# Kernel tuning notes

Measured on AMD Instinct MI355X. Metric: run time of the kernel, lower is better.

## Reference

```python
import jax, jax.numpy as jnp
import numpy as np
import math

D_INNER = 512
D_STATE = 16
DT_RANK = 32
B_SZ = 2
L_SEQ = 4096


def setup_inputs() -> dict:
    key = jax.random.key(0)
    ks = jax.random.split(key, 6)
    x = jax.random.normal(ks[0], (B_SZ, L_SEQ, D_INNER), dtype=jnp.float32)
    # parameters (match torch init semantics closely enough for a numeric baseline)
    A = jnp.arange(1, D_STATE + 1, dtype=jnp.float32)
    A_log = jnp.broadcast_to(jnp.log(A)[None, :], (D_INNER, D_STATE)).copy()
    D_param = jnp.ones((D_INNER,), dtype=jnp.float32)
    # x_proj: Linear(d_inner -> dt_rank + 2*d_state), no bias
    W_xproj = jax.random.normal(ks[1], (DT_RANK + 2 * D_STATE, D_INNER), dtype=jnp.float32) / np.sqrt(D_INNER)
    # dt_proj: Linear(dt_rank -> d_inner) with special bias init
    W_dt = jax.random.normal(ks[2], (D_INNER, DT_RANK), dtype=jnp.float32) / np.sqrt(DT_RANK)
    dt_init = jnp.exp(jax.random.uniform(ks[3], (D_INNER,)) * (math.log(0.1) - math.log(0.001)) + math.log(0.001))
    b_dt = jnp.log(jnp.exp(dt_init) - 1.0)
    alpha = jnp.asarray(0.6, dtype=jnp.float32)
    beta_logit = jnp.asarray(math.log(0.99 / (1.0 - 0.99 + 1e-08)), dtype=jnp.float32)
    return {"x": x, "A_log": A_log, "D_param": D_param, "W_xproj": W_xproj,
            "W_dt": W_dt, "b_dt": b_dt, "alpha": alpha, "beta_logit": beta_logit}


def _momentum_ssm(x, A_log, D_param, W_xproj, W_dt, b_dt, alpha, beta_logit):
    # x: (B, L, D)
    proj = jnp.einsum('bld,pd->blp', x, W_xproj)            # (B, L, r+2N)
    dt_in = proj[..., :DT_RANK]
    Bp = proj[..., DT_RANK:DT_RANK + D_STATE]                # (B, L, N)
    Cp = proj[..., DT_RANK + D_STATE:]                       # (B, L, N)
    dt = jax.nn.softplus(jnp.einsum('blr,dr->bld', dt_in, W_dt) + b_dt)  # (B, L, D)
    A = -jnp.exp(A_log)                                      # (D, N)
    A_bar = jnp.exp(dt[..., None] * A[None, None])           # (B, L, D, N)
    # fused B_bar * x_t: dt * Bp * x
    inp = dt[..., None] * Bp[:, :, None, :] * x[..., None]   # (B, L, D, N)
    beta = jax.nn.sigmoid(beta_logit)

    # scan over time; carry (h, v): (B, D, N)
    h0 = jnp.zeros((x.shape[0], D_INNER, D_STATE), dtype=x.dtype)
    v0 = jnp.zeros_like(h0)

    def step(carry, ts):
        h, v = carry
        a_t, inp_t, c_t = ts                                 # (B,D,N), (B,D,N), (B,N)
        v = beta * v + alpha * inp_t
        h = a_t * h + v
        y = jnp.einsum('bdn,bn->bd', h, c_t)
        return (h, v), y

    xs = (jnp.moveaxis(A_bar, 1, 0), jnp.moveaxis(inp, 1, 0), jnp.moveaxis(Cp, 1, 0))
    _, ys = jax.lax.scan(step, (h0, v0), xs)                 # ys: (L, B, D)
    y = jnp.moveaxis(ys, 0, 1)                               # (B, L, D)
    return y + D_param * x


def reference(x, A_log, D_param, W_xproj, W_dt, b_dt, alpha, beta_logit):
    return _momentum_ssm(x, A_log, D_param, W_xproj, W_dt, b_dt, alpha, beta_logit)
```

## Files before the change

kernel.cpp:

```cpp
#include <hip/hip_runtime.h>


#define D_IN 512
#define D_ST 16
#define DTR  32
#define BSZ  2
#define LSEQ 4096
#define PDIM 64
#define NCH  256
#define LCH  (LSEQ / NCH)
#define LOG2E 1.44269504f
#define LN2   0.69314718f

typedef __attribute__((ext_vector_type(8))) short short8;
typedef __attribute__((ext_vector_type(4))) float f32x4;
typedef _Float16 f16;
typedef __attribute__((ext_vector_type(8))) _Float16 f16x8;

__device__ inline float fast_exp2(float x) { return __builtin_amdgcn_exp2f(x); }
__device__ inline float fast_log2(float x) { return __builtin_amdgcn_logf(x); }

__device__ inline unsigned short bf16_rne(float f) {
  unsigned b = __float_as_uint(f);
  return (unsigned short)((b + 0x7fffu + ((b >> 16) & 1u)) >> 16);
}

__device__ inline void cvt8(const float4 u, const float4 v, short8& hi, short8& lo) {
  float f[8] = {u.x, u.y, u.z, u.w, v.x, v.y, v.z, v.w};
#pragma unroll
  for (int i = 0; i < 8; ++i) {
    unsigned short h = bf16_rne(f[i]);
    hi[i] = (short)h;
    float r = f[i] - __uint_as_float((unsigned)h << 16);
    lo[i] = (short)bf16_rne(r);
  }
}

__device__ inline void st16h(f16* p, const float* s) {
  f16 t[16];
#pragma unroll
  for (int i = 0; i < 16; ++i) t[i] = (f16)s[i];
  *(f16x8*)p = *(f16x8*)&t[0];
  *(f16x8*)(p + 8) = *(f16x8*)&t[8];
}
__device__ inline void ld16h(const f16* p, float* d) {
  f16x8 a = *(const f16x8*)p;
  f16x8 b = *(const f16x8*)(p + 8);
#pragma unroll
  for (int i = 0; i < 8; ++i) { d[i] = (float)a[i]; d[8 + i] = (float)b[i]; }
}

__device__ inline bool loadA2(const float* A_log, int d, float* A2) {
  const float4* ap = (const float4*)(A_log + (size_t)d * D_ST);
#pragma unroll
  for (int i = 0; i < 4; ++i) {
    float4 a4 = ap[i];
    A2[4 * i + 0] = -__expf(a4.x) * LOG2E;
    A2[4 * i + 1] = -__expf(a4.y) * LOG2E;
    A2[4 * i + 2] = -__expf(a4.z) * LOG2E;
    A2[4 * i + 3] = -__expf(a4.w) * LOG2E;
  }
  bool pw = true;
#pragma unroll
  for (int n = 1; n < 16; ++n) {
    float ref = (float)(n + 1) * A2[0];
    pw = pw && (fabsf(A2[n] - ref) <= 2e-5f * fabsf(ref));
  }
  return pw;
}

__global__ __launch_bounds__(256) void k_wprep(const float* __restrict__ W,
                                               short* __restrict__ Whi,
                                               short* __restrict__ Wlo) {
  const int i = (blockIdx.x * 256 + threadIdx.x) * 4;
  float4 w = *(const float4*)(W + i);
  float f[4] = {w.x, w.y, w.z, w.w};
  unsigned short h[4], lo[4];
#pragma unroll
  for (int j = 0; j < 4; ++j) {
    h[j] = bf16_rne(f[j]);
    float r = f[j] - __uint_as_float((unsigned)h[j] << 16);
    lo[j] = bf16_rne(r);
  }
  *(uint2*)(Whi + i) = make_uint2(h[0] | ((unsigned)h[1] << 16), h[2] | ((unsigned)h[3] << 16));
  *(uint2*)(Wlo + i) = make_uint2(lo[0] | ((unsigned)lo[1] << 16), lo[2] | ((unsigned)lo[3] << 16));
}

#define MM3(ACC, AH, AL, BH, BL)                                        \
  ACC = __builtin_amdgcn_mfma_f32_16x16x32_bf16(AL, BH, ACC, 0, 0, 0);  \
  ACC = __builtin_amdgcn_mfma_f32_16x16x32_bf16(AH, BL, ACC, 0, 0, 0);  \
  ACC = __builtin_amdgcn_mfma_f32_16x16x32_bf16(AH, BH, ACC, 0, 0, 0);

#define LOADB(P, S)                                   \
  {                                                   \
    const int kb = ((S) & 15) * 32;                   \
    P##h0 = *(const short8*)(bh + kb);                \
    P##h1 = *(const short8*)(bh + 8192 + kb);         \
    P##h2 = *(const short8*)(bh + 16384 + kb);        \
    P##h3 = *(const short8*)(bh + 24576 + kb);        \
    P##l0 = *(const short8*)(bl + kb);                \
    P##l1 = *(const short8*)(bl + 8192 + kb);         \
    P##l2 = *(const short8*)(bl + 16384 + kb);        \
    P##l3 = *(const short8*)(bl + 24576 + kb);        \
  }

#define LOADA(Aa, Ab, S)                              \
  {                                                   \
    const int ka = ((S) & 15) * 32;                   \
    Aa = *(const float4*)(xr + ka);                   \
    Ab = *(const float4*)(xr + ka + 4);               \
  }

#define SUBSTEP(Aa, Ab, P, SA, SB)                    \
  {                                                   \
    short8 ahi, alo;                                  \
    cvt8(Aa, Ab, ahi, alo);                           \
    MM3(acc0, ahi, alo, P##h0, P##l0);                \
    MM3(acc1, ahi, alo, P##h1, P##l1);                \
    MM3(acc2, ahi, alo, P##h2, P##l2);                \
    MM3(acc3, ahi, alo, P##h3, P##l3);                \
    LOADB(P, SB);                                     \
    LOADA(Aa, Ab, SA);                                \
  }

__global__ __launch_bounds__(64) void k_proj(const float* __restrict__ x,
                                             const short* __restrict__ Whi,
                                             const short* __restrict__ Wlo,
                                             float* __restrict__ proj) {
  const int row0 = blockIdx.x * 16;
  const int l = threadIdx.x;
  const int m = l & 15;
  const int ko = (l >> 4) * 8;
  const float* xr = x + (size_t)(row0 + m) * D_IN + ko;
  const short* bh = Whi + (size_t)m * D_IN + ko;
  const short* bl = Wlo + (size_t)m * D_IN + ko;

  f32x4 acc0 = {0.f, 0.f, 0.f, 0.f}, acc1 = acc0, acc2 = acc0, acc3 = acc0;
  float4 A0a, A0b, A1a, A1b, A2a, A2b, A3a, A3b;
  short8 Xh0, Xh1, Xh2, Xh3, Xl0, Xl1, Xl2, Xl3;
  short8 Yh0, Yh1, Yh2, Yh3, Yl0, Yl1, Yl2, Yl3;
  LOADA(A0a, A0b, 0); LOADA(A1a, A1b, 1); LOADA(A2a, A2b, 2); LOADA(A3a, A3b, 3);
  LOADB(X, 0); LOADB(Y, 1);

#pragma unroll
  for (int it = 0; it < 4; ++it) {
    const int s = it * 4;
    SUBSTEP(A0a, A0b, X, s + 4, s + 2);
    SUBSTEP(A1a, A1b, Y, s + 5, s + 3);
    SUBSTEP(A2a, A2b, X, s + 6, s + 4);
    SUBSTEP(A3a, A3b, Y, s + 7, s + 5);
  }

  const int r0 = (l >> 4) * 4;
#pragma unroll
  for (int r = 0; r < 4; ++r) {
    float* pr = proj + (size_t)(row0 + r0 + r) * PDIM + m;
    pr[0] = acc0[r]; pr[16] = acc1[r]; pr[32] = acc2[r]; pr[48] = acc3[r];
  }
}

#define S1_BODY(GET_A)                                        \
  _Pragma("unroll")                                           \
  for (int j = 0; j < LCH; ++j) {                             \
    const float dtc = dtv[j], xv = xs[j];                     \
    sd += dtc;                                                \
    bpow *= beta;                                             \
    const float u = alpha * dtc * xv;                         \
    GET_A;                                                    \
    float4 Bq[4];                                             \
    _Pragma("unroll")                                         \
    for (int i = 0; i < 4; ++i) Bq[i] = ((const float4*)&Ps[j][DTR])[i]; \
    const float* Bf = (const float*)Bq;                       \
    float ar = 1.f;                                           \
    _Pragma("unroll")                                         \
    for (int n = 0; n < 16; ++n) {                            \
      NEXT_A(ar, n);                                          \
      v[n] = fmaf(beta, v[n], u * Bf[n]);                     \
      h[n] = fmaf(ar, h[n], v[n]);                            \
      cv[n] = fmaf(ar, cv[n], bpow);                          \
    }                                                         \
  }

__global__ __launch_bounds__(256) void k_scan1(const float* __restrict__ x,
                                               const float* __restrict__ proj,
                                               const float* __restrict__ A_log,
                                               const float* __restrict__ W_dt,
                                               const float* __restrict__ b_dt,
                                               const float* __restrict__ alpha_p,
                                               const float* __restrict__ beta_p,
                                               f16* __restrict__ hh,
                                               f16* __restrict__ vh,
                                               f16* __restrict__ cvv,
                                               float* __restrict__ sdt,
                                               f16* __restrict__ dth) {
  __shared__ float Ps[LCH][PDIM];
  const int c = blockIdx.x, b = blockIdx.z;
  const int d = blockIdx.y * 256 + threadIdx.x;
  const int t0 = c * LCH;
  {
    const float4* src = (const float4*)(proj + ((size_t)b * LSEQ + t0) * PDIM);
    ((float4*)&Ps[0][0])[threadIdx.x] = src[threadIdx.x];
  }
  float xs[LCH];
  {
    const float* xp = x + ((size_t)b * LSEQ + t0) * D_IN + d;
#pragma unroll
    for (int j = 0; j < LCH; ++j) xs[j] = xp[(size_t)j * D_IN];
  }
  const float alpha = alpha_p[0];
  const float beta = 1.f / (1.f + __expf(-beta_p[0]));
  float A2[D_ST];
  const bool powA = loadA2(A_log, d, A2);
  __syncthreads();

  float dtv[LCH];
  {
    float4 w4[8];
    const float4* wp = (const float4*)(W_dt + (size_t)d * DTR);
#pragma unroll
    for (int i = 0; i < 8; ++i) w4[i] = wp[i];
    const float bb = b_dt[d];
#pragma unroll
    for (int j = 0; j < LCH; ++j) {
      const float4* pj = (const float4*)&Ps[j][0];
      float a0 = bb, a1 = 0.f, a2 = 0.f, a3 = 0.f;
#pragma unroll
      for (int k = 0; k < 8; ++k) {
        float4 p = pj[k];
        a0 = fmaf(p.x, w4[k].x, a0);
        a1 = fmaf(p.y, w4[k].y, a1);
        a2 = fmaf(p.z, w4[k].z, a2);
        a3 = fmaf(p.w, w4[k].w, a3);
      }
      float acc = (a0 + a1) + (a2 + a3);
      float e = fast_exp2(acc * LOG2E);
      dtv[j] = (acc > 20.f) ? acc : LN2 * fast_log2(1.f + e);
    }
  }
  {
    f16* dp = dth + ((size_t)b * LSEQ + t0) * D_IN + d;
#pragma unroll
    for (int j = 0; j < LCH; ++j) dp[(size_t)j * D_IN] = (f16)dtv[j];
  }

  float h[16] = {}, v[16] = {}, cv[16] = {};
  float bpow = 1.f, sd = 0.f;
  if (powA) {
#define NEXT_A(ar, n) ar *= r
    S1_BODY(const float r = fast_exp2(dtc * A2[0]))
#undef NEXT_A
  } else {
#define NEXT_A(ar, n) ar = fast_exp2(dtc * A2[n])
    S1_BODY()
#undef NEXT_A
  }

  const size_t base = ((size_t)(b * NCH + c) * D_IN + d) * D_ST;
  st16h(hh + base, h);
  st16h(vh + base, v);
  st16h(cvv + base, cv);
  sdt[(size_t)(b * NCH + c) * D_IN + d] = sd;
}

__global__ __launch_bounds__(64) void k_fix(f16* __restrict__ hh,
                                            f16* __restrict__ vh,
                                            const f16* __restrict__ cvv,
                                            const float* __restrict__ sdt,
                                            const float* __restrict__ A_log,
                                            const float* __restrict__ beta_p) {
  const int g = blockIdx.x * 64 + threadIdx.x;
  const int b = g >> 13;
  const int dn = g & 8191;
  const float beta = 1.f / (1.f + __expf(-beta_p[0]));
  const float A2 = -__expf(A_log[dn]) * LOG2E;
  float bL = beta;
#pragma unroll
  for (int i = 0; i < 4; ++i) bL *= bL;

  const size_t cs = (size_t)D_IN * D_ST;
  const size_t base = (size_t)b * NCH * cs + dn;
  const size_t sbase = (size_t)b * NCH * D_IN + (dn >> 4);

  float hg[8], vg[8], cg[8], sg[8];
#pragma unroll
  for (int i = 0; i < 8; ++i) {
    hg[i] = (float)hh[base + i * cs];
    vg[i] = (float)vh[base + i * cs];
    cg[i] = (float)cvv[base + i * cs];
    sg[i] = sdt[sbase + i * D_IN];
  }
  float H = 0.f, V = 0.f;
  for (int c0 = 0; c0 < NCH; c0 += 8) {
    const int cp = (c0 + 8) & (NCH - 1);
    float hn[8], vn[8], cn[8], sn[8];
#pragma unroll
    for (int i = 0; i < 8; ++i) {
      hn[i] = (float)hh[base + (size_t)(cp + i) * cs];
      vn[i] = (float)vh[base + (size_t)(cp + i) * cs];
      cn[i] = (float)cvv[base + (size_t)(cp + i) * cs];
      sn[i] = sdt[sbase + (size_t)(cp + i) * D_IN];
    }
#pragma unroll
    for (int i = 0; i < 8; ++i) {
      hh[base + (size_t)(c0 + i) * cs] = (f16)H;
      vh[base + (size_t)(c0 + i) * cs] = (f16)V;
      const float Pa = fast_exp2(sg[i] * A2);
      const float Hn = fmaf(Pa, H, fmaf(cg[i], V, hg[i]));
      V = fmaf(bL, V, vg[i]);
      H = Hn;
    }
#pragma unroll
    for (int i = 0; i < 8; ++i) { hg[i] = hn[i]; vg[i] = vn[i]; cg[i] = cn[i]; sg[i] = sn[i]; }
  }
}

#define S2_BODY(GET_A)                                        \
  _Pragma("unroll")                                           \
  for (int j = 0; j < LCH; ++j) {                             \
    const float dtc = dtv[j], xv = xs[j];                     \
    const float u = alpha * dtc * xv;                         \
    GET_A;                                                    \
    float4 Bq[8];                                             \
    _Pragma("unroll")                                         \
    for (int i = 0; i < 8; ++i) Bq[i] = ((const float4*)&Ps[j][DTR])[i]; \
    const float* Bf = (const float*)Bq;                       \
    float y0 = 0.f, y1 = 0.f, y2 = 0.f, y3 = 0.f;             \
    float ar = 1.f;                                           \
    _Pragma("unroll")                                         \
    for (int n = 0; n < 16; ++n) {                            \
      NEXT_A(ar, n);                                          \
      v[n] = fmaf(beta, v[n], u * Bf[n]);                     \
      h[n] = fmaf(ar, h[n], v[n]);                            \
      float hc = h[n] * Bf[16 + n];                           \
      if ((n & 3) == 0) y0 += hc;                             \
      else if ((n & 3) == 1) y1 += hc;                        \
      else if ((n & 3) == 2) y2 += hc;                        \
      else y3 += hc;                                          \
    }                                                         \
    op[(size_t)j * D_IN] = (y0 + y1) + (y2 + y3) + Dv * xv;   \
  }

__global__ __launch_bounds__(256) void k_scan2(const float* __restrict__ x,
                                               const f16* __restrict__ dth,
                                               const float* __restrict__ proj,
                                               const float* __restrict__ A_log,
                                               const float* __restrict__ D_param,
                                               const float* __restrict__ alpha_p,
                                               const float* __restrict__ beta_p,
                                               const f16* __restrict__ hh,
                                               const f16* __restrict__ vh,
                                               float* __restrict__ out) {
  __shared__ float Ps[LCH][PDIM];
  const int c = blockIdx.x, b = blockIdx.z;
  const int d = blockIdx.y * 256 + threadIdx.x;
  const int t0 = c * LCH;
  {
    const float4* src = (const float4*)(proj + ((size_t)b * LSEQ + t0) * PDIM);
    ((float4*)&Ps[0][0])[threadIdx.x] = src[threadIdx.x];
  }
  float xs[LCH], dtv[LCH];
  {
    const float* xp = x + ((size_t)b * LSEQ + t0) * D_IN + d;
    const f16* dp = dth + ((size_t)b * LSEQ + t0) * D_IN + d;
#pragma unroll
    for (int j = 0; j < LCH; ++j) xs[j] = xp[(size_t)j * D_IN];
#pragma unroll
    for (int j = 0; j < LCH; ++j) dtv[j] = (float)dp[(size_t)j * D_IN];
  }
  const float alpha = alpha_p[0];
  const float beta = 1.f / (1.f + __expf(-beta_p[0]));
  const float Dv = D_param[d];
  float A2[D_ST];
  const bool powA = loadA2(A_log, d, A2);
  const size_t ibase = ((size_t)(b * NCH + c) * D_IN + d) * D_ST;
  float h[16], v[16];
  ld16h(hh + ibase, h);
  ld16h(vh + ibase, v);
  __syncthreads();

  float* op = out + ((size_t)b * LSEQ + t0) * D_IN + d;
  if (powA) {
#define NEXT_A(ar, n) ar *= r
    S2_BODY(const float r = fast_exp2(dtc * A2[0]))
#undef NEXT_A
  } else {
#define NEXT_A(ar, n) ar = fast_exp2(dtc * A2[n])
    S2_BODY()
#undef NEXT_A
  }
}

extern "C" void kernel_launch(void* const* d_in, const int* in_sizes, int n_in,
                              void* d_out, int out_size, void* d_ws, size_t ws_size,
                              hipStream_t stream) {
  const float* x = (const float*)d_in[0];
  const float* A_log = (const float*)d_in[1];
  const float* D_param = (const float*)d_in[2];
  const float* W_xproj = (const float*)d_in[3];
  const float* W_dt = (const float*)d_in[4];
  const float* b_dt = (const float*)d_in[5];
  const float* alpha = (const float*)d_in[6];
  const float* beta_logit = (const float*)d_in[7];
  float* out = (float*)d_out;

  const size_t NST = (size_t)BSZ * NCH * D_IN * D_ST;
  float* ws = (float*)d_ws;
  float* proj = ws;
  float* sdt = proj + (size_t)BSZ * LSEQ * PDIM;
  f16* hh = (f16*)(sdt + (size_t)BSZ * NCH * D_IN);
  f16* vh = hh + NST;
  f16* cvv = vh + NST;
  f16* dth = cvv + NST;
  short* Whi = (short*)(dth + (size_t)BSZ * LSEQ * D_IN);
  short* Wlo = Whi + (size_t)PDIM * D_IN;

  k_wprep<<<dim3(PDIM * D_IN / 1024), dim3(256), 0, stream>>>(W_xproj, Whi, Wlo);
  k_proj<<<dim3(BSZ * LSEQ / 16), dim3(64), 0, stream>>>(x, Whi, Wlo, proj);
  k_scan1<<<dim3(NCH, D_IN / 256, BSZ), dim3(256), 0, stream>>>(
      x, proj, A_log, W_dt, b_dt, alpha, beta_logit, hh, vh, cvv, sdt, dth);
  k_fix<<<dim3(BSZ * D_IN * D_ST / 64), dim3(64), 0, stream>>>(hh, vh, cvv, sdt, A_log,
                                                               beta_logit);
  k_scan2<<<dim3(NCH, D_IN / 256, BSZ), dim3(256), 0, stream>>>(
      x, dth, proj, A_log, D_param, alpha, beta_logit, hh, vh, out);
}
```

Baseline: 172.5 us.

## Move dt projection into a separate MFMA kernel with split-bf16 weights

The dt = softplus(dt_in·W_dtᵀ + b) computation moves out of the scan1 per-thread FMA loop into a new k_dt kernel. That kernel uses bf16 hi/lo split MFMAs, with W_dt prepared in k_wprep. scan1 now reads dt from the f16 buffer, and both scans stage only the B/C columns into smaller shared arrays, with launch bounds asking for 4 blocks per CU. This removes the scalar GEMV work from the latency-bound scan and may raise occupancy. In exchange it adds a kernel launch plus a global write and read of dt.

```diff
diff --git a/kernel.cpp b/kernel.cpp
--- a/kernel.cpp
+++ b/kernel.cpp
@@ -17,6 +17,9 @@
 typedef _Float16 f16;
 typedef __attribute__((ext_vector_type(8))) _Float16 f16x8;
 
+__device__ __align__(16) short g_Wdh[D_IN * DTR];
+__device__ __align__(16) short g_Wdl[D_IN * DTR];
+
 __device__ inline float fast_exp2(float x) { return __builtin_amdgcn_exp2f(x); }
 __device__ inline float fast_log2(float x) { return __builtin_amdgcn_logf(x); }
 
@@ -70,10 +73,19 @@
 }
 
 __global__ __launch_bounds__(256) void k_wprep(const float* __restrict__ W,
+                                               const float* __restrict__ Wdt,
                                                short* __restrict__ Whi,
                                                short* __restrict__ Wlo) {
   const int i = (blockIdx.x * 256 + threadIdx.x) * 4;
-  float4 w = *(const float4*)(W + i);
+  const float* src;
+  short *dh, *dl;
+  if (i < PDIM * D_IN) {
+    src = W + i; dh = Whi + i; dl = Wlo + i;
+  } else {
+    const int k = i - PDIM * D_IN;
+    src = Wdt + k; dh = g_Wdh + k; dl = g_Wdl + k;
+  }
+  float4 w = *(const float4*)src;
   float f[4] = {w.x, w.y, w.z, w.w};
   unsigned short h[4], lo[4];
 #pragma unroll
@@ -82,8 +94,8 @@
     float r = f[j] - __uint_as_float((unsigned)h[j] << 16);
     lo[j] = bf16_rne(r);
   }
-  *(uint2*)(Whi + i) = make_uint2(h[0] | ((unsigned)h[1] << 16), h[2] | ((unsigned)h[3] << 16));
-  *(uint2*)(Wlo + i) = make_uint2(lo[0] | ((unsigned)lo[1] << 16), lo[2] | ((unsigned)lo[3] << 16));
+  *(uint2*)dh = make_uint2(h[0] | ((unsigned)h[1] << 16), h[2] | ((unsigned)h[3] << 16));
+  *(uint2*)dl = make_uint2(lo[0] | ((unsigned)lo[1] << 16), lo[2] | ((unsigned)lo[3] << 16));
 }
 
 #define MM3(ACC, AH, AL, BH, BL)                                        \
@@ -159,6 +171,56 @@
   }
 }
 
+__global__ __launch_bounds__(64) void k_dt(const float* __restrict__ proj,
+                                           const float* __restrict__ b_dt,
+                                           f16* __restrict__ dth) {
+  const int row0 = blockIdx.x * 16;
+  const int col0 = blockIdx.y * 64;
+  const int l = threadIdx.x;
+  const int m = l & 15;
+  const int ko = (l >> 4) * 8;
+  const float* ap = proj + (size_t)(row0 + m) * PDIM + ko;
+  const short* bh = g_Wdh + (col0 + m) * DTR + ko;
+  const short* bl = g_Wdl + (col0 + m) * DTR + ko;
+
+  float4 Aa = *(const float4*)ap;
+  float4 Ab = *(const float4*)(ap + 4);
+  short8 ahi, alo;
+  cvt8(Aa, Ab, ahi, alo);
+  short8 B0h = *(const short8*)bh;
+  short8 B1h = *(const short8*)(bh + 16 * DTR);
+  short8 B2h = *(const short8*)(bh + 32 * DTR);
+  short8 B3h = *(const short8*)(bh + 48 * DTR);
+  short8 B0l = *(const short8*)bl;
+  short8 B1l = *(const short8*)(bl + 16 * DTR);
+  short8 B2l = *(const short8*)(bl + 32 * DTR);
+  short8 B3l = *(const short8*)(bl + 48 * DTR);
+
+  f32x4 acc0 = {0.f, 0.f, 0.f, 0.f}, acc1 = acc0, acc2 = acc0, acc3 = acc0;
+  MM3(acc0, ahi, alo, B0h, B0l);
+  MM3(acc1, ahi, alo, B1h, B1l);
+  MM3(acc2, ahi, alo, B2h, B2l);
+  MM3(acc3, ahi, alo, B3h, B3l);
+
+  float bb[4];
+#pragma unroll
+  for (int cc = 0; cc < 4; ++cc) bb[cc] = b_dt[col0 + m + 16 * cc];
+
+  const int r0 = (l >> 4) * 4;
+#pragma unroll
+  for (int r = 0; r < 4; ++r) {
+    const size_t t = (size_t)(row0 + r0 + r);
+    float vals[4] = {acc0[r], acc1[r], acc2[r], acc3[r]};
+#pragma unroll
+    for (int cc = 0; cc < 4; ++cc) {
+      float a = vals[cc] + bb[cc];
+      float e = fast_exp2(a * LOG2E);
+      float dt = (a > 20.f) ? a : LN2 * fast_log2(1.f + e);
+      dth[t * D_IN + col0 + m + 16 * cc] = (f16)dt;
+    }
+  }
+}
+
 #define S1_BODY(GET_A)                                        \
   _Pragma("unroll")                                           \
   for (int j = 0; j < LCH; ++j) {                             \
@@ -169,7 +231,7 @@
     GET_A;                                                    \
     float4 Bq[4];                                             \
     _Pragma("unroll")                                         \
-    for (int i = 0; i < 4; ++i) Bq[i] = ((const float4*)&Ps[j][DTR])[i]; \
+    for (int i = 0; i < 4; ++i) Bq[i] = ((const float4*)&Ps[j][0])[i]; \
     const float* Bf = (const float*)Bq;                       \
     float ar = 1.f;                                           \
     _Pragma("unroll")                                         \
@@ -181,67 +243,39 @@
     }                                                         \
   }
 
-__global__ __launch_bounds__(256) void k_scan1(const float* __restrict__ x,
-                                               const float* __restrict__ proj,
-                                               const float* __restrict__ A_log,
-                                               const float* __restrict__ W_dt,
-                                               const float* __restrict__ b_dt,
-                                               const float* __restrict__ alpha_p,
-                                               const float* __restrict__ beta_p,
-                                               f16* __restrict__ hh,
-                                               f16* __restrict__ vh,
-                                               f16* __restrict__ cvv,
-                                               float* __restrict__ sdt,
-                                               f16* __restrict__ dth) {
-  __shared__ float Ps[LCH][PDIM];
+__global__ __launch_bounds__(256, 4) void k_scan1(const float* __restrict__ x,
+                                                  const f16* __restrict__ dth,
+                                                  const float* __restrict__ proj,
+                                                  const float* __restrict__ A_log,
+                                                  const float* __restrict__ alpha_p,
+                                                  const float* __restrict__ beta_p,
+                                                  f16* __restrict__ hh,
+                                                  f16* __restrict__ vh,
+                                                  f16* __restrict__ cvv,
+                                                  float* __restrict__ sdt) {
+  __shared__ float Ps[LCH][D_ST];
   const int c = blockIdx.x, b = blockIdx.z;
   const int d = blockIdx.y * 256 + threadIdx.x;
   const int t0 = c * LCH;
-  {
+  if (threadIdx.x < 64) {
     const float4* src = (const float4*)(proj + ((size_t)b * LSEQ + t0) * PDIM);
-    ((float4*)&Ps[0][0])[threadIdx.x] = src[threadIdx.x];
-  }
-  float xs[LCH];
+    ((float4*)&Ps[0][0])[threadIdx.x] =
+        src[(threadIdx.x >> 2) * (PDIM / 4) + (DTR / 4) + (threadIdx.x & 3)];
+  }
+  float xs[LCH], dtv[LCH];
   {
     const float* xp = x + ((size_t)b * LSEQ + t0) * D_IN + d;
+    const f16* dp = dth + ((size_t)b * LSEQ + t0) * D_IN + d;
 #pragma unroll
     for (int j = 0; j < LCH; ++j) xs[j] = xp[(size_t)j * D_IN];
+#pragma unroll
+    for (int j = 0; j < LCH; ++j) dtv[j] = (float)dp[(size_t)j * D_IN];
   }
   const float alpha = alpha_p[0];
   const float beta = 1.f / (1.f + __expf(-beta_p[0]));
   float A2[D_ST];
   const bool powA = loadA2(A_log, d, A2);
   __syncthreads();
-
-  float dtv[LCH];
-  {
-    float4 w4[8];
-    const float4* wp = (const float4*)(W_dt + (size_t)d * DTR);
-#pragma unroll
-    for (int i = 0; i < 8; ++i) w4[i] = wp[i];
-    const float bb = b_dt[d];
-#pragma unroll
-    for (int j = 0; j < LCH; ++j) {
-      const float4* pj = (const float4*)&Ps[j][0];
-      float a0 = bb, a1 = 0.f, a2 = 0.f, a3 = 0.f;
-#pragma unroll
-      for (int k = 0; k < 8; ++k) {
-        float4 p = pj[k];
-        a0 = fmaf(p.x, w4[k].x, a0);
-        a1 = fmaf(p.y, w4[k].y, a1);
-        a2 = fmaf(p.z, w4[k].z, a2);
-        a3 = fmaf(p.w, w4[k].w, a3);
-      }
-      float acc = (a0 + a1) + (a2 + a3);
-      float e = fast_exp2(acc * LOG2E);
-      dtv[j] = (acc > 20.f) ? acc : LN2 * fast_log2(1.f + e);
-    }
-  }
-  {
-    f16* dp = dth + ((size_t)b * LSEQ + t0) * D_IN + d;
-#pragma unroll
-    for (int j = 0; j < LCH; ++j) dp[(size_t)j * D_IN] = (f16)dtv[j];
-  }
 
   float h[16] = {}, v[16] = {}, cv[16] = {};
   float bpow = 1.f, sd = 0.f;
@@ -322,7 +356,7 @@
     GET_A;                                                    \
     float4 Bq[8];                                             \
     _Pragma("unroll")                                         \
-    for (int i = 0; i < 8; ++i) Bq[i] = ((const float4*)&Ps[j][DTR])[i]; \
+    for (int i = 0; i < 8; ++i) Bq[i] = ((const float4*)&Ps[j][0])[i]; \
     const float* Bf = (const float*)Bq;                       \
     float y0 = 0.f, y1 = 0.f, y2 = 0.f, y3 = 0.f;             \
     float ar = 1.f;                                           \
@@ -340,23 +374,24 @@
     op[(size_t)j * D_IN] = (y0 + y1) + (y2 + y3) + Dv * xv;   \
   }
 
-__global__ __launch_bounds__(256) void k_scan2(const float* __restrict__ x,
-                                               const f16* __restrict__ dth,
-                                               const float* __restrict__ proj,
-                                               const float* __restrict__ A_log,
-                                               const float* __restrict__ D_param,
-                                               const float* __restrict__ alpha_p,
-                                               const float* __restrict__ beta_p,
-                                               const f16* __restrict__ hh,
-                                               const f16* __restrict__ vh,
-                                               float* __restrict__ out) {
-  __shared__ float Ps[LCH][PDIM];
+__global__ __launch_bounds__(256, 4) void k_scan2(const float* __restrict__ x,
+                                                  const f16* __restrict__ dth,
+                                                  const float* __restrict__ proj,
+                                                  const float* __restrict__ A_log,
+                                                  const float* __restrict__ D_param,
+                                                  const float* __restrict__ alpha_p,
+                                                  const float* __restrict__ beta_p,
+                                                  const f16* __restrict__ hh,
+                                                  const f16* __restrict__ vh,
+                                                  float* __restrict__ out) {
+  __shared__ float Ps[LCH][2 * D_ST];
   const int c = blockIdx.x, b = blockIdx.z;
   const int d = blockIdx.y * 256 + threadIdx.x;
   const int t0 = c * LCH;
-  {
+  if (threadIdx.x < 128) {
     const float4* src = (const float4*)(proj + ((size_t)b * LSEQ + t0) * PDIM);
-    ((float4*)&Ps[0][0])[threadIdx.x] = src[threadIdx.x];
+    ((float4*)&Ps[0][0])[threadIdx.x] =
+        src[(threadIdx.x >> 3) * (PDIM / 4) + (DTR / 4) + (threadIdx.x & 7)];
   }
   float xs[LCH], dtv[LCH];
   {
@@ -414,10 +449,12 @@
   short* Whi = (short*)(dth + (size_t)BSZ * LSEQ * D_IN);
   short* Wlo = Whi + (size_t)PDIM * D_IN;
 
-  k_wprep<<<dim3(PDIM * D_IN / 1024), dim3(256), 0, stream>>>(W_xproj, Whi, Wlo);
+  k_wprep<<<dim3((PDIM * D_IN + D_IN * DTR) / 1024), dim3(256), 0, stream>>>(
+      W_xproj, W_dt, Whi, Wlo);
   k_proj<<<dim3(BSZ * LSEQ / 16), dim3(64), 0, stream>>>(x, Whi, Wlo, proj);
+  k_dt<<<dim3(BSZ * LSEQ / 16, D_IN / 64), dim3(64), 0, stream>>>(proj, b_dt, dth);
   k_scan1<<<dim3(NCH, D_IN / 256, BSZ), dim3(256), 0, stream>>>(
-      x, proj, A_log, W_dt, b_dt, alpha, beta_logit, hh, vh, cvv, sdt, dth);
+      x, dth, proj, A_log, alpha, beta_logit, hh, vh, cvv, sdt);
   k_fix<<<dim3(BSZ * D_IN * D_ST / 64), dim3(64), 0, stream>>>(hh, vh, cvv, sdt, A_log,
                                                                beta_logit);
   k_scan2<<<dim3(NCH, D_IN / 256, BSZ), dim3(256), 0, stream>>>(
```

Result: slower. 209.3 us (+21.4%).

## Split scan1 state dimension across two threads per channel

Applied to the files above, without the earlier changes.

k_scan1 now assigns two threads to each d channel, with each thread handling 8 of the 16 state entries. This doubles the grid and cuts per-thread register pressure, and launch bounds now request 4 blocks per CU to raise occupancy. The cost is duplicated work: both threads load x, compute the dt projection and softplus, and the upper-half thread raises r to the 8th power to seed its A-power chain. The per-step dependency chain also gets shorter, so latency should be easier to hide.

```diff
diff --git a/kernel.cpp b/kernel.cpp
--- a/kernel.cpp
+++ b/kernel.cpp
@@ -36,12 +36,11 @@
   }
 }
 
-__device__ inline void st16h(f16* p, const float* s) {
-  f16 t[16];
-#pragma unroll
-  for (int i = 0; i < 16; ++i) t[i] = (f16)s[i];
+__device__ inline void st8h(f16* p, const float* s) {
+  f16 t[8];
+#pragma unroll
+  for (int i = 0; i < 8; ++i) t[i] = (f16)s[i];
   *(f16x8*)p = *(f16x8*)&t[0];
-  *(f16x8*)(p + 8) = *(f16x8*)&t[8];
 }
 __device__ inline void ld16h(const f16* p, float* d) {
   f16x8 a = *(const f16x8*)p;
@@ -66,6 +65,30 @@
     float ref = (float)(n + 1) * A2[0];
     pw = pw && (fabsf(A2[n] - ref) <= 2e-5f * fabsf(ref));
   }
+  return pw;
+}
+
+__device__ inline bool loadA2half(const float* A_log, int d, int hf, float* A2h,
+                                  float& a0) {
+  const float4* ap = (const float4*)(A_log + (size_t)d * D_ST);
+  float t[16];
+#pragma unroll
+  for (int i = 0; i < 4; ++i) {
+    float4 a4 = ap[i];
+    t[4 * i + 0] = -__expf(a4.x) * LOG2E;
+    t[4 * i + 1] = -__expf(a4.y) * LOG2E;
+    t[4 * i + 2] = -__expf(a4.z) * LOG2E;
+    t[4 * i + 3] = -__expf(a4.w) * LOG2E;
+  }
+  a0 = t[0];
+  bool pw = true;
+#pragma unroll
+  for (int n = 1; n < 16; ++n) {
+    float ref = (float)(n + 1) * t[0];
+    pw = pw && (fabsf(t[n] - ref) <= 2e-5f * fabsf(ref));
+  }
+#pragma unroll
+  for (int k = 0; k < 8; ++k) A2h[k] = t[8 * hf + k];
   return pw;
 }
 
@@ -159,43 +182,22 @@
   }
 }
 
-#define S1_BODY(GET_A)                                        \
-  _Pragma("unroll")                                           \
-  for (int j = 0; j < LCH; ++j) {                             \
-    const float dtc = dtv[j], xv = xs[j];                     \
-    sd += dtc;                                                \
-    bpow *= beta;                                             \
-    const float u = alpha * dtc * xv;                         \
-    GET_A;                                                    \
-    float4 Bq[4];                                             \
-    _Pragma("unroll")                                         \
-    for (int i = 0; i < 4; ++i) Bq[i] = ((const float4*)&Ps[j][DTR])[i]; \
-    const float* Bf = (const float*)Bq;                       \
-    float ar = 1.f;                                           \
-    _Pragma("unroll")                                         \
-    for (int n = 0; n < 16; ++n) {                            \
-      NEXT_A(ar, n);                                          \
-      v[n] = fmaf(beta, v[n], u * Bf[n]);                     \
-      h[n] = fmaf(ar, h[n], v[n]);                            \
-      cv[n] = fmaf(ar, cv[n], bpow);                          \
-    }                                                         \
-  }
-
-__global__ __launch_bounds__(256) void k_scan1(const float* __restrict__ x,
-                                               const float* __restrict__ proj,
-                                               const float* __restrict__ A_log,
-                                               const float* __restrict__ W_dt,
-                                               const float* __restrict__ b_dt,
-                                               const float* __restrict__ alpha_p,
-                                               const float* __restrict__ beta_p,
-                                               f16* __restrict__ hh,
-                                               f16* __restrict__ vh,
-                                               f16* __restrict__ cvv,
-                                               float* __restrict__ sdt,
-                                               f16* __restrict__ dth) {
+__global__ __launch_bounds__(256, 4) void k_scan1(const float* __restrict__ x,
+                                                  const float* __restrict__ proj,
+                                                  const float* __restrict__ A_log,
+                                                  const float* __restrict__ W_dt,
+                                                  const float* __restrict__ b_dt,
+                                                  const float* __restrict__ alpha_p,
+                                                  const float* __restrict__ beta_p,
+                                                  f16* __restrict__ hh,
+                                                  f16* __restrict__ vh,
+                                                  f16* __restrict__ cvv,
+                                                  float* __restrict__ sdt,
+                                                  f16* __restrict__ dth) {
   __shared__ float Ps[LCH][PDIM];
   const int c = blockIdx.x, b = blockIdx.z;
-  const int d = blockIdx.y * 256 + threadIdx.x;
+  const int hf = threadIdx.x & 1;
+  const int d = blockIdx.y * 128 + (threadIdx.x >> 1);
   const int t0 = c * LCH;
   {
     const float4* src = (const float4*)(proj + ((size_t)b * LSEQ + t0) * PDIM);
@@ -209,8 +211,8 @@
   }
   const float alpha = alpha_p[0];
   const float beta = 1.f / (1.f + __expf(-beta_p[0]));
-  float A2[D_ST];
-  const bool powA = loadA2(A_log, d, A2);
+  float A2h[8], a0;
+  const bool powA = loadA2half(A_log, d, hf, A2h, a0);
   __syncthreads();
 
   float dtv[LCH];
@@ -223,43 +225,78 @@
 #pragma unroll
     for (int j = 0; j < LCH; ++j) {
       const float4* pj = (const float4*)&Ps[j][0];
-      float a0 = bb, a1 = 0.f, a2 = 0.f, a3 = 0.f;
+      float c0 = bb, c1 = 0.f, c2 = 0.f, c3 = 0.f;
 #pragma unroll
       for (int k = 0; k < 8; ++k) {
         float4 p = pj[k];
-        a0 = fmaf(p.x, w4[k].x, a0);
-        a1 = fmaf(p.y, w4[k].y, a1);
-        a2 = fmaf(p.z, w4[k].z, a2);
-        a3 = fmaf(p.w, w4[k].w, a3);
+        c0 = fmaf(p.x, w4[k].x, c0);
+        c1 = fmaf(p.y, w4[k].y, c1);
+        c2 = fmaf(p.z, w4[k].z, c2);
+        c3 = fmaf(p.w, w4[k].w, c3);
       }
-      float acc = (a0 + a1) + (a2 + a3);
+      float acc = (c0 + c1) + (c2 + c3);
       float e = fast_exp2(acc * LOG2E);
       dtv[j] = (acc > 20.f) ? acc : LN2 * fast_log2(1.f + e);
     }
   }
-  {
+  if (hf == 0) {
     f16* dp = dth + ((size_t)b * LSEQ + t0) * D_IN + d;
 #pragma unroll
     for (int j = 0; j < LCH; ++j) dp[(size_t)j * D_IN] = (f16)dtv[j];
   }
 
-  float h[16] = {}, v[16] = {}, cv[16] = {};
+  float h8[8] = {}, v8[8] = {}, cv8[8] = {};
   float bpow = 1.f, sd = 0.f;
   if (powA) {
-#define NEXT_A(ar, n) ar *= r
-    S1_BODY(const float r = fast_exp2(dtc * A2[0]))
-#undef NEXT_A
+#pragma unroll
+    for (int j = 0; j < LCH; ++j) {
+      const float dtc = dtv[j], xv = xs[j];
+      sd += dtc;
+      bpow *= beta;
+      const float u = alpha * dtc * xv;
+      const float r = fast_exp2(dtc * a0);
+      float ar = 1.f;
+      if (hf) {
+        const float r2 = r * r;
+        const float r4 = r2 * r2;
+        ar = r4 * r4;
+      }
+      float4 B0 = *(const float4*)&Ps[j][DTR + 8 * hf];
+      float4 B1 = *(const float4*)&Ps[j][DTR + 8 * hf + 4];
+      const float Bf[8] = {B0.x, B0.y, B0.z, B0.w, B1.x, B1.y, B1.z, B1.w};
+#pragma unroll
+      for (int k = 0; k < 8; ++k) {
+        ar *= r;
+        v8[k] = fmaf(beta, v8[k], u * Bf[k]);
+        h8[k] = fmaf(ar, h8[k], v8[k]);
+        cv8[k] = fmaf(ar, cv8[k], bpow);
+      }
+    }
   } else {
-#define NEXT_A(ar, n) ar = fast_exp2(dtc * A2[n])
-    S1_BODY()
-#undef NEXT_A
-  }
-
-  const size_t base = ((size_t)(b * NCH + c) * D_IN + d) * D_ST;
-  st16h(hh + base, h);
-  st16h(vh + base, v);
-  st16h(cvv + base, cv);
-  sdt[(size_t)(b * NCH + c) * D_IN + d] = sd;
+#pragma unroll
+    for (int j = 0; j < LCH; ++j) {
+      const float dtc = dtv[j], xv = xs[j];
+      sd += dtc;
+      bpow *= beta;
+      const float u = alpha * dtc * xv;
+      float4 B0 = *(const float4*)&Ps[j][DTR + 8 * hf];
+      float4 B1 = *(const float4*)&Ps[j][DTR + 8 * hf + 4];
+      const float Bf[8] = {B0.x, B0.y, B0.z, B0.w, B1.x, B1.y, B1.z, B1.w};
+#pragma unroll
+      for (int k = 0; k < 8; ++k) {
+        const float ar = fast_exp2(dtc * A2h[k]);
+        v8[k] = fmaf(beta, v8[k], u * Bf[k]);
+        h8[k] = fmaf(ar, h8[k], v8[k]);
+        cv8[k] = fmaf(ar, cv8[k], bpow);
+      }
+    }
+  }
+
+  const size_t base = ((size_t)(b * NCH + c) * D_IN + d) * D_ST + hf * 8;
+  st8h(hh + base, h8);
+  st8h(vh + base, v8);
+  st8h(cvv + base, cv8);
+  if (hf == 0) sdt[(size_t)(b * NCH + c) * D_IN + d] = sd;
 }
 
 __global__ __launch_bounds__(64) void k_fix(f16* __restrict__ hh,
@@ -416,7 +453,7 @@
 
   k_wprep<<<dim3(PDIM * D_IN / 1024), dim3(256), 0, stream>>>(W_xproj, Whi, Wlo);
   k_proj<<<dim3(BSZ * LSEQ / 16), dim3(64), 0, stream>>>(x, Whi, Wlo, proj);
-  k_scan1<<<dim3(NCH, D_IN / 256, BSZ), dim3(256), 0, stream>>>(
+  k_scan1<<<dim3(NCH, D_IN / 128, BSZ), dim3(256), 0, stream>>>(
       x, proj, A_log, W_dt, b_dt, alpha, beta_logit, hh, vh, cvv, sdt, dth);
   k_fix<<<dim3(BSZ * D_IN * D_ST / 64), dim3(64), 0, stream>>>(hh, vh, cvv, sdt, A_log,
                                                                beta_logit);
```

Measured after the change: 208.4 us. 20.8% more time.

## Split each channel's scan1 state across two lanes and interleave dt computation

Applied to the files above, without the earlier changes.

k_scan1 now gives each (d) channel two threads, each handling 8 of the 16 state dimensions and half of the dt_proj dot product, combined with a shuffle. The dt softplus is computed inline per timestep instead of in a separate pre-pass, and the power-of-A path starts the second half at r^8. This doubles the thread count and cuts per-thread registers and serial work, at the cost of redundant x loads, a shuffle per step and duplicated softplus evaluation.

```diff
diff --git a/kernel.cpp b/kernel.cpp
--- a/kernel.cpp
+++ b/kernel.cpp
@@ -36,12 +36,11 @@
   }
 }
 
-__device__ inline void st16h(f16* p, const float* s) {
-  f16 t[16];
-#pragma unroll
-  for (int i = 0; i < 16; ++i) t[i] = (f16)s[i];
+__device__ inline void st8h(f16* p, const float* s) {
+  f16 t[8];
+#pragma unroll
+  for (int i = 0; i < 8; ++i) t[i] = (f16)s[i];
   *(f16x8*)p = *(f16x8*)&t[0];
-  *(f16x8*)(p + 8) = *(f16x8*)&t[8];
 }
 __device__ inline void ld16h(const f16* p, float* d) {
   f16x8 a = *(const f16x8*)p;
@@ -159,26 +158,44 @@
   }
 }
 
-#define S1_BODY(GET_A)                                        \
-  _Pragma("unroll")                                           \
-  for (int j = 0; j < LCH; ++j) {                             \
-    const float dtc = dtv[j], xv = xs[j];                     \
-    sd += dtc;                                                \
-    bpow *= beta;                                             \
-    const float u = alpha * dtc * xv;                         \
-    GET_A;                                                    \
-    float4 Bq[4];                                             \
-    _Pragma("unroll")                                         \
-    for (int i = 0; i < 4; ++i) Bq[i] = ((const float4*)&Ps[j][DTR])[i]; \
-    const float* Bf = (const float*)Bq;                       \
-    float ar = 1.f;                                           \
-    _Pragma("unroll")                                         \
-    for (int n = 0; n < 16; ++n) {                            \
-      NEXT_A(ar, n);                                          \
-      v[n] = fmaf(beta, v[n], u * Bf[n]);                     \
-      h[n] = fmaf(ar, h[n], v[n]);                            \
-      cv[n] = fmaf(ar, cv[n], bpow);                          \
-    }                                                         \
+
+#define PWCHK(val, n)                                                        \
+  pw = pw && (fabsf((val) - (float)((n) + 1) * a0) <=                        \
+              2e-5f * fabsf((float)((n) + 1) * a0));
+
+#define S1_LOOP                                                              \
+  _Pragma("unroll")                                                          \
+  for (int j = 0; j < LCH; ++j) {                                            \
+    const float4* pj = (const float4*)&Ps[j][16 * hf];                       \
+    float c0 = 0.f, c1 = 0.f, c2 = 0.f, c3 = 0.f;                            \
+    _Pragma("unroll")                                                        \
+    for (int k = 0; k < 4; ++k) {                                            \
+      float4 p = pj[k];                                                      \
+      c0 = fmaf(p.x, w4[k].x, c0);                                           \
+      c1 = fmaf(p.y, w4[k].y, c1);                                           \
+      c2 = fmaf(p.z, w4[k].z, c2);                                           \
+      c3 = fmaf(p.w, w4[k].w, c3);                                           \
+    }                                                                        \
+    const float part = (c0 + c1) + (c2 + c3);                                \
+    const float acc = part + __shfl_xor(part, 1, 64) + bb;                   \
+    const float ee = fast_exp2(acc * LOG2E);                                 \
+    const float dtc = (acc > 20.f) ? acc : LN2 * fast_log2(1.f + ee);        \
+    if (hf == 0) dp[(size_t)j * D_IN] = (f16)dtc;                            \
+    sd += dtc;                                                               \
+    bpow *= beta;                                                            \
+    const float xv = xs[j];                                                  \
+    const float u = alpha * dtc * xv;                                        \
+    float4 B0 = *(const float4*)&Ps[j][DTR + 8 * hf];                        \
+    float4 B1 = *(const float4*)&Ps[j][DTR + 8 * hf + 4];                    \
+    const float Bf[8] = {B0.x, B0.y, B0.z, B0.w, B1.x, B1.y, B1.z, B1.w};    \
+    AR_INIT;                                                                 \
+    _Pragma("unroll")                                                        \
+    for (int k = 0; k < 8; ++k) {                                            \
+      AR_STEP;                                                               \
+      v8[k] = fmaf(beta, v8[k], u * Bf[k]);                                  \
+      h8[k] = fmaf(ar, h8[k], v8[k]);                                        \
+      cv8[k] = fmaf(ar, cv8[k], bpow);                                       \
+    }                                                                        \
   }
 
 __global__ __launch_bounds__(256) void k_scan1(const float* __restrict__ x,
@@ -195,7 +212,8 @@
                                                f16* __restrict__ dth) {
   __shared__ float Ps[LCH][PDIM];
   const int c = blockIdx.x, b = blockIdx.z;
-  const int d = blockIdx.y * 256 + threadIdx.x;
+  const int hf = threadIdx.x & 1;
+  const int d = blockIdx.y * 128 + (threadIdx.x >> 1);
   const int t0 = c * LCH;
   {
     const float4* src = (const float4*)(proj + ((size_t)b * LSEQ + t0) * PDIM);
@@ -207,59 +225,71 @@
 #pragma unroll
     for (int j = 0; j < LCH; ++j) xs[j] = xp[(size_t)j * D_IN];
   }
+  float4 w4[4];
+  {
+    const float4* wp = (const float4*)(W_dt + (size_t)d * DTR + 16 * hf);
+#pragma unroll
+    for (int i = 0; i < 4; ++i) w4[i] = wp[i];
+  }
+  const float bb = b_dt[d];
   const float alpha = alpha_p[0];
   const float beta = 1.f / (1.f + __expf(-beta_p[0]));
-  float A2[D_ST];
-  const bool powA = loadA2(A_log, d, A2);
+
+  float4 e0, e1, e2, e3;
+  {
+    const float4* ap = (const float4*)(A_log + (size_t)d * D_ST);
+    float4 r0 = ap[0], r1 = ap[1], r2 = ap[2], r3 = ap[3];
+    e0 = make_float4(-__expf(r0.x) * LOG2E, -__expf(r0.y) * LOG2E,
+                     -__expf(r0.z) * LOG2E, -__expf(r0.w) * LOG2E);
+    e1 = make_float4(-__expf(r1.x) * LOG2E, -__expf(r1.y) * LOG2E,
+                     -__expf(r1.z) * LOG2E, -__expf(r1.w) * LOG2E);
+    e2 = make_float4(-__expf(r2.x) * LOG2E, -__expf(r2.y) * LOG2E,
+                     -__expf(r2.z) * LOG2E, -__expf(r2.w) * LOG2E);
+    e3 = make_float4(-__expf(r3.x) * LOG2E, -__expf(r3.y) * LOG2E,
+                     -__expf(r3.z) * LOG2E, -__expf(r3.w) * LOG2E);
+  }
+  const float a0 = e0.x;
+  bool pw = true;
+  PWCHK(e0.y, 1) PWCHK(e0.z, 2) PWCHK(e0.w, 3)
+  PWCHK(e1.x, 4) PWCHK(e1.y, 5) PWCHK(e1.z, 6) PWCHK(e1.w, 7)
+  PWCHK(e2.x, 8) PWCHK(e2.y, 9) PWCHK(e2.z, 10) PWCHK(e2.w, 11)
+  PWCHK(e3.x, 12) PWCHK(e3.y, 13) PWCHK(e3.z, 14) PWCHK(e3.w, 15)
+  float A2h[8];
+  {
+    float4 u0 = hf ? e2 : e0;
+    float4 u1 = hf ? e3 : e1;
+    A2h[0] = u0.x; A2h[1] = u0.y; A2h[2] = u0.z; A2h[3] = u0.w;
+    A2h[4] = u1.x; A2h[5] = u1.y; A2h[6] = u1.z; A2h[7] = u1.w;
+  }
   __syncthreads();
 
-  float dtv[LCH];
-  {
-    float4 w4[8];
-    const float4* wp = (const float4*)(W_dt + (size_t)d * DTR);
-#pragma unroll
-    for (int i = 0; i < 8; ++i) w4[i] = wp[i];
-    const float bb = b_dt[d];
-#pragma unroll
-    for (int j = 0; j < LCH; ++j) {
-      const float4* pj = (const float4*)&Ps[j][0];
-      float a0 = bb, a1 = 0.f, a2 = 0.f, a3 = 0.f;
-#pragma unroll
-      for (int k = 0; k < 8; ++k) {
-        float4 p = pj[k];
-        a0 = fmaf(p.x, w4[k].x, a0);
-        a1 = fmaf(p.y, w4[k].y, a1);
-        a2 = fmaf(p.z, w4[k].z, a2);
-        a3 = fmaf(p.w, w4[k].w, a3);
-      }
-      float acc = (a0 + a1) + (a2 + a3);
-      float e = fast_exp2(acc * LOG2E);
-      dtv[j] = (acc > 20.f) ? acc : LN2 * fast_log2(1.f + e);
-    }
-  }
-  {
-    f16* dp = dth + ((size_t)b * LSEQ + t0) * D_IN + d;
-#pragma unroll
-    for (int j = 0; j < LCH; ++j) dp[(size_t)j * D_IN] = (f16)dtv[j];
-  }
-
-  float h[16] = {}, v[16] = {}, cv[16] = {};
+  f16* dp = dth + ((size_t)b * LSEQ + t0) * D_IN + d;
+  float h8[8] = {}, v8[8] = {}, cv8[8] = {};
   float bpow = 1.f, sd = 0.f;
-  if (powA) {
-#define NEXT_A(ar, n) ar *= r
-    S1_BODY(const float r = fast_exp2(dtc * A2[0]))
-#undef NEXT_A
+
+  if (pw) {
+#define AR_INIT                                                   \
+    const float r = fast_exp2(dtc * a0);                          \
+    const float r2 = r * r;                                       \
+    const float r4 = r2 * r2;                                     \
+    float ar = hf ? r4 * r4 : 1.f
+#define AR_STEP ar *= r
+    S1_LOOP
+#undef AR_INIT
+#undef AR_STEP
   } else {
-#define NEXT_A(ar, n) ar = fast_exp2(dtc * A2[n])
-    S1_BODY()
-#undef NEXT_A
-  }
-
-  const size_t base = ((size_t)(b * NCH + c) * D_IN + d) * D_ST;
-  st16h(hh + base, h);
-  st16h(vh + base, v);
-  st16h(cvv + base, cv);
-  sdt[(size_t)(b * NCH + c) * D_IN + d] = sd;
+#define AR_INIT float ar
+#define AR_STEP ar = fast_exp2(dtc * A2h[k])
+    S1_LOOP
+#undef AR_INIT
+#undef AR_STEP
+  }
+
+  const size_t base = ((size_t)(b * NCH + c) * D_IN + d) * D_ST + hf * 8;
+  st8h(hh + base, h8);
+  st8h(vh + base, v8);
+  st8h(cvv + base, cv8);
+  if (hf == 0) sdt[(size_t)(b * NCH + c) * D_IN + d] = sd;
 }
 
 __global__ __launch_bounds__(64) void k_fix(f16* __restrict__ hh,
@@ -416,7 +446,7 @@
 
   k_wprep<<<dim3(PDIM * D_IN / 1024), dim3(256), 0, stream>>>(W_xproj, Whi, Wlo);
   k_proj<<<dim3(BSZ * LSEQ / 16), dim3(64), 0, stream>>>(x, Whi, Wlo, proj);
-  k_scan1<<<dim3(NCH, D_IN / 256, BSZ), dim3(256), 0, stream>>>(
+  k_scan1<<<dim3(NCH, D_IN / 128, BSZ), dim3(256), 0, stream>>>(
       x, proj, A_log, W_dt, b_dt, alpha, beta_logit, hh, vh, cvv, sdt, dth);
   k_fix<<<dim3(BSZ * D_IN * D_ST / 64), dim3(64), 0, stream>>>(hh, vh, cvv, sdt, A_log,
                                                                beta_logit);
```

Result: slower. 176.0 us (+2.0%).
